# Kernel tuning notes

Hardware: AMD Instinct MI355X
Metric: run time of the kernel (lower is better)

The kernel has to match this reference:

```python
import math
import jax, jax.numpy as jnp
import numpy as np

BASE = 10000.0
SCALING_FACTOR = 1.0
ORIG_MAX_POS = 4096
BETA_FAST, BETA_SLOW = 32, 1
MSCALE = 0.707
MSCALE_ALL_DIM = 0.707


def _yarn_cos_sin(seq_len: int, dim: int):
    # DeepseekV3YarnRotaryEmbedding._set_cos_sin_cache, computed in numpy (constants)
    def corr_dim(num_rot):
        return dim * math.log(ORIG_MAX_POS / (num_rot * 2 * math.pi)) / (2 * math.log(BASE))
    low = max(math.floor(corr_dim(BETA_FAST)), 0)
    high = min(math.ceil(corr_dim(BETA_SLOW)), dim - 1)
    hi = high + 0.001 if low == high else high
    ramp = np.clip((np.arange(dim // 2, dtype=np.float32) - low) / (hi - low), 0.0, 1.0)
    inv_freq_mask = 1.0 - ramp
    freq_extra = 1.0 / BASE ** (np.arange(0, dim, 2, dtype=np.float32) / dim)
    freq_inter = freq_extra / SCALING_FACTOR
    inv_freq = freq_inter * (1.0 - inv_freq_mask) + freq_extra * inv_freq_mask
    t = np.arange(seq_len, dtype=np.float32)
    freqs = np.outer(t, inv_freq)
    def get_mscale(s, m):
        return 1.0 if s <= 1 else 0.1 * m * math.log(s) + 1.0
    _m = get_mscale(SCALING_FACTOR, MSCALE) / get_mscale(SCALING_FACTOR, MSCALE_ALL_DIM)
    emb = np.concatenate([freqs, freqs], axis=-1)  # [S, dim]
    return jnp.asarray(np.cos(emb) * _m), jnp.asarray(np.sin(emb) * _m)


def _rotate_half(x):
    x1, x2 = jnp.split(x, 2, axis=-1)
    return jnp.concatenate([-x2, x1], axis=-1)


def setup_inputs() -> dict:
    key = jax.random.key(0)
    ks = jax.random.split(key, 5)
    B, S, H, DN, DR, DV = 2, 2048, 16, 128, 64, 128
    return {
        "q_nope": jax.random.normal(ks[0], (B, S, H, DN), jnp.float32),
        "q_pe": jax.random.normal(ks[1], (B, S, H, DR), jnp.float32),
        "k_nope": jax.random.normal(ks[2], (B, S, H, DN), jnp.float32),
        "k_pe": jax.random.normal(ks[3], (B, S, 1, DR), jnp.float32),  # shared rope key head
        "v": jax.random.normal(ks[4], (B, S, H, DV), jnp.float32),
    }


def reference(q_nope, q_pe, k_nope, k_pe, v):
    B, S, H, DN = q_nope.shape
    DR = q_pe.shape[-1]
    sm_scale = (DN + DR) ** (-0.5)  # qk_head_dim**-0.5
    cos, sin = _yarn_cos_sin(S, DR)  # [S, DR]
    cos = cos[None, :, None, :]
    sin = sin[None, :, None, :]
    # decoupled RoPE on the rope slice (apply_rotary_pos_emb with position_ids=arange)
    qp = q_pe * cos + _rotate_half(q_pe) * sin              # [B,S,H,DR]
    kp = k_pe * cos + _rotate_half(k_pe) * sin              # [B,S,1,DR]
    kp = jnp.broadcast_to(kp, (B, S, H, DR))
    q = jnp.concatenate([q_nope, qp], axis=-1)              # [B,S,H,DN+DR]
    k = jnp.concatenate([k_nope, kp], axis=-1)
    # attention_ref: full fp32 logits, causal mask, lse*log2(e), softmax, PV
    logits = jnp.einsum('bmhd,bnhd->bhmn', q.astype(jnp.float32), k.astype(jnp.float32)) * sm_scale
    mask = jnp.arange(S)[:, None] >= jnp.arange(S)[None, :]  # qo_len == kv_len
    logits = jnp.where(mask[None, None], logits, -jnp.inf)
    lse = jnp.transpose(jax.scipy.special.logsumexp(logits, axis=-1), (0, 2, 1)) * math.log2(math.e)
    p = jax.nn.softmax(logits, axis=-1)
    o = jnp.einsum('bhmn,bnhd->bmhd', p, v.astype(jnp.float32))
    o = o.reshape(B * S, H, -1).astype(q_nope.dtype)        # [B*S, H, DV]
    return o, lse
```

## Files before the change

kernel.cpp:

```cpp
#include <hip/hip_runtime.h>
#include <hip/hip_bf16.h>
#include <math.h>

#define NB 2
#define SEQ 2048
#define NH 16
#define DNOPE 128
#define DROT 64
#define DVDIM 128
#define DQK 192
#define BM 64
#define BN 64

typedef __bf16 bf16x8_t __attribute__((ext_vector_type(8)));
typedef float f32x4_t __attribute__((ext_vector_type(4)));

#define LOG2_BASE_OVER_HALFDIM 0.41524101186092028f
#define KSL2 0.10412340175817158f

#define KBF_ELEMS   ((size_t)NB * NH * SEQ * DQK)
#define KPREP_BLOCKS 6144
#define VPREP_BLOCKS 1024

__global__ __launch_bounds__(256) void prep_kernel(
    const float* __restrict__ k_nope, const float* __restrict__ k_pe,
    const float* __restrict__ v, __bf16* __restrict__ Kbf,
    __bf16* __restrict__ Vtb) {
  __shared__ __bf16 T[64][130];
  const int bid = blockIdx.x;
  const int tid = threadIdx.x;
  if (bid < KPREP_BLOCKS) {
    int gid = bid * 256 + tid;
    size_t o8 = (size_t)gid * 8;
    int d0 = (int)(o8 % DQK);
    int rest = (int)(o8 / DQK);
    int s = rest & (SEQ - 1);
    int bh = rest >> 11;
    int h = bh & (NH - 1), b = bh >> 4;
    bf16x8_t o;
    if (d0 < DNOPE) {
      const float* p = k_nope + ((size_t)((b * SEQ + s) * NH + h)) * DNOPE + d0;
      float4 a = *(const float4*)p;
      float4 c = *(const float4*)(p + 4);
      o[0] = (__bf16)a.x; o[1] = (__bf16)a.y; o[2] = (__bf16)a.z; o[3] = (__bf16)a.w;
      o[4] = (__bf16)c.x; o[5] = (__bf16)c.y; o[6] = (__bf16)c.z; o[7] = (__bf16)c.w;
    } else {
      int dr0 = d0 - DNOPE;
      const float* p = k_pe + (size_t)(b * SEQ + s) * DROT;
#pragma unroll
      for (int j = 0; j < 8; ++j) {
        int dr = dr0 + j;
        int i = dr & 31;
        float invf = exp2f(-LOG2_BASE_OVER_HALFDIM * (float)i);
        float ang = (float)s * invf;
        float sn, cs; sincosf(ang, &sn, &cs);
        float x = p[dr];
        float oth = (dr < 32) ? -p[dr + 32] : p[dr - 32];
        o[j] = (__bf16)(x * cs + oth * sn);
      }
    }
    *(bf16x8_t*)&Kbf[o8] = o;
  } else {
    int vb = bid - KPREP_BLOCKS;
    const int s0 = (vb & 31) * 64, h = (vb >> 5) & (NH - 1), b = vb >> 9;
#pragma unroll
    for (int r = 0; r < 8; ++r) {
      int task = tid + r * 256;
      int srow = task >> 5, c4 = (task & 31) * 4;
      const float* p = v + ((size_t)((b * SEQ + s0 + srow) * NH + h)) * DVDIM + c4;
      float4 a = *(const float4*)p;
      T[srow][c4 + 0] = (__bf16)a.x; T[srow][c4 + 1] = (__bf16)a.y;
      T[srow][c4 + 2] = (__bf16)a.z; T[srow][c4 + 3] = (__bf16)a.w;
    }
    __syncthreads();
#pragma unroll
    for (int r = 0; r < 4; ++r) {
      int task = tid + r * 256;
      int dv = task >> 3, c8 = (task & 7) * 8;
      bf16x8_t o;
#pragma unroll
      for (int u = 0; u < 8; ++u) o[u] = T[c8 + u][dv];
      *(bf16x8_t*)&Vtb[((size_t)(b * NH + h) * DVDIM + dv) * SEQ + s0 + c8] = o;
    }
  }
}

__global__ __launch_bounds__(256, 2) void mla_fwd_kernel(
    const float* __restrict__ q_nope, const float* __restrict__ q_pe,
    const __bf16* __restrict__ Kbf, const __bf16* __restrict__ Vtb,
    float* __restrict__ out_o, float* __restrict__ out_lse) {
  __shared__ __bf16 Kl[BN * DQK];
  __shared__ __bf16 Vl[DVDIM * BN];
  __shared__ __bf16 Pl[4 * 16 * BN];
  __shared__ __bf16 Vx[16 * 72];

  const int bx = blockIdx.x, h = blockIdx.y, b = blockIdx.z;
  const int tid = threadIdx.x;
  const int w = tid >> 6, lane = tid & 63;
  const int col = lane & 15, quad = lane >> 4;
  const int swz = col & 7;
  const int e0 = quad ^ swz, e1 = (quad + 4) ^ swz;

  for (int i = tid; i < 16 * 72; i += 256)
    Vx[i] = (i < 64) ? (__bf16)1.0f : (__bf16)0.0f;

  const __bf16* Kslab = Kbf + (size_t)(b * NH + h) * SEQ * DQK;
  const __bf16* Vslab = Vtb + (size_t)(b * NH + h) * DVDIM * SEQ;

  int kofs[6];
#pragma unroll
  for (int r = 0; r < 6; ++r) {
    int L = r * 256 + tid;
    int n = L / 24, jj = L - n * 24;
    int jsrc = (jj & ~7) | ((jj & 7) ^ (n & 7));
    kofs[r] = n * DQK + jsrc * 8;
  }
  int vofs[4];
#pragma unroll
  for (int r = 0; r < 4; ++r) {
    int L = r * 256 + tid;
    int dv = L >> 3, jj = L & 7;
    vofs[r] = dv * SEQ + (jj ^ (dv & 7)) * 8;
  }

  __syncthreads();
  const bf16x8_t vxf0 = *(const bf16x8_t*)&Vx[col * 72 + quad * 8];
  const bf16x8_t vxf1 = *(const bf16x8_t*)&Vx[col * 72 + 32 + quad * 8];

  for (int half = 0; half < 2; ++half) {
    const int qt = half ? bx : (31 - bx);
    const int qb = qt * BM;
    const int mrow = qb + w * 16 + col;

    const float* qn = q_nope + (size_t)((b * SEQ + mrow) * NH + h) * DNOPE;
    const float* qp = q_pe   + (size_t)((b * SEQ + mrow) * NH + h) * DROT;
    bf16x8_t qfrag[6];
#pragma unroll
    for (int c = 0; c < 4; ++c) {
      const float* p = qn + c * 32 + quad * 8;
      float4 a = *(const float4*)p;
      float4 bq = *(const float4*)(p + 4);
      bf16x8_t f;
      f[0]=(__bf16)(a.x*KSL2);  f[1]=(__bf16)(a.y*KSL2);
      f[2]=(__bf16)(a.z*KSL2);  f[3]=(__bf16)(a.w*KSL2);
      f[4]=(__bf16)(bq.x*KSL2); f[5]=(__bf16)(bq.y*KSL2);
      f[6]=(__bf16)(bq.z*KSL2); f[7]=(__bf16)(bq.w*KSL2);
      qfrag[c] = f;
    }
    {
      const float* plo = qp + quad * 8;
      const float* phi = qp + 32 + quad * 8;
      float4 lo0 = *(const float4*)plo;
      float4 lo1 = *(const float4*)(plo + 4);
      float4 hi0 = *(const float4*)phi;
      float4 hi1 = *(const float4*)(phi + 4);
      float xl[8] = {lo0.x,lo0.y,lo0.z,lo0.w,lo1.x,lo1.y,lo1.z,lo1.w};
      float xh[8] = {hi0.x,hi0.y,hi0.z,hi0.w,hi1.x,hi1.y,hi1.z,hi1.w};
      bf16x8_t f4v, f5v;
#pragma unroll
      for (int j = 0; j < 8; ++j) {
        int i = quad * 8 + j;
        float invf = exp2f(-LOG2_BASE_OVER_HALFDIM * (float)i);
        float ang = (float)mrow * invf;
        float sn, cs; sincosf(ang, &sn, &cs);
        f4v[j] = (__bf16)((xl[j] * cs - xh[j] * sn) * KSL2);
        f5v[j] = (__bf16)((xh[j] * cs + xl[j] * sn) * KSL2);
      }
      qfrag[4] = f4v; qfrag[5] = f5v;
    }

    f32x4_t oacc[8];
#pragma unroll
    for (int i = 0; i < 8; ++i) oacc[i] = (f32x4_t){0.f, 0.f, 0.f, 0.f};
    f32x4_t lacc = (f32x4_t){0.f, 0.f, 0.f, 0.f};
    float m_run[4] = {-INFINITY, -INFINITY, -INFINITY, -INFINITY};

    bf16x8_t Kreg[6], Vreg[4];
#pragma unroll
    for (int r = 0; r < 6; ++r) Kreg[r] = *(const bf16x8_t*)(Kslab + kofs[r]);
#pragma unroll
    for (int r = 0; r < 4; ++r) Vreg[r] = *(const bf16x8_t*)(Vslab + vofs[r]);

    for (int it = 0; it <= qt; ++it) {
      __syncthreads();
#pragma unroll
      for (int r = 0; r < 6; ++r) *(bf16x8_t*)&Kl[(r * 256 + tid) * 8] = Kreg[r];
#pragma unroll
      for (int r = 0; r < 4; ++r) *(bf16x8_t*)&Vl[(r * 256 + tid) * 8] = Vreg[r];
      __syncthreads();
      if (it < qt) {
        const __bf16* Ksrc = Kslab + (size_t)(it + 1) * BN * DQK;
        const __bf16* Vsrc = Vslab + (it + 1) * BN;
#pragma unroll
        for (int r = 0; r < 6; ++r) Kreg[r] = *(const bf16x8_t*)(Ksrc + kofs[r]);
#pragma unroll
        for (int r = 0; r < 4; ++r) Vreg[r] = *(const bf16x8_t*)(Vsrc + vofs[r]);
      }

      f32x4_t sacc[4];
#pragma unroll
      for (int t = 0; t < 4; ++t) sacc[t] = (f32x4_t){0.f, 0.f, 0.f, 0.f};
#pragma unroll
      for (int t = 0; t < 4; ++t) {
        const __bf16* kr = &Kl[(t * 16 + col) * 24 * 8];
        sacc[t] = __builtin_amdgcn_mfma_f32_16x16x32_bf16(qfrag[0], *(const bf16x8_t*)&kr[e0 * 8], sacc[t], 0, 0, 0);
        sacc[t] = __builtin_amdgcn_mfma_f32_16x16x32_bf16(qfrag[1], *(const bf16x8_t*)&kr[e1 * 8], sacc[t], 0, 0, 0);
        sacc[t] = __builtin_amdgcn_mfma_f32_16x16x32_bf16(qfrag[2], *(const bf16x8_t*)&kr[64 + e0 * 8], sacc[t], 0, 0, 0);
        sacc[t] = __builtin_amdgcn_mfma_f32_16x16x32_bf16(qfrag[3], *(const bf16x8_t*)&kr[64 + e1 * 8], sacc[t], 0, 0, 0);
        sacc[t] = __builtin_amdgcn_mfma_f32_16x16x32_bf16(qfrag[4], *(const bf16x8_t*)&kr[128 + e0 * 8], sacc[t], 0, 0, 0);
        sacc[t] = __builtin_amdgcn_mfma_f32_16x16x32_bf16(qfrag[5], *(const bf16x8_t*)&kr[128 + e1 * 8], sacc[t], 0, 0, 0);
      }

      const bool diag = (it == qt);
      float pv[4][4];
      float alpha[4];
#pragma unroll
      for (int r = 0; r < 4; ++r) {
        float mx = -INFINITY;
#pragma unroll
        for (int t = 0; t < 4; ++t) {
          float sv = sacc[t][r];
          if (diag) {
            int nn = (qt << 6) + t * 16 + col;
            int mm = qb + w * 16 + quad * 4 + r;
            if (nn > mm) sv = -INFINITY;
          }
          pv[t][r] = sv;
          mx = fmaxf(mx, sv);
        }
        mx = fmaxf(mx, __shfl_xor(mx, 1, 64));
        mx = fmaxf(mx, __shfl_xor(mx, 2, 64));
        mx = fmaxf(mx, __shfl_xor(mx, 4, 64));
        mx = fmaxf(mx, __shfl_xor(mx, 8, 64));
        float mnew = fmaxf(m_run[r], mx);
        alpha[r] = exp2f(m_run[r] - mnew);
        m_run[r] = mnew;
#pragma unroll
        for (int t = 0; t < 4; ++t) pv[t][r] = exp2f(pv[t][r] - mnew);
      }
#pragma unroll
      for (int d = 0; d < 8; ++d) {
        f32x4_t o = oacc[d];
        o[0] *= alpha[0]; o[1] *= alpha[1]; o[2] *= alpha[2]; o[3] *= alpha[3];
        oacc[d] = o;
      }
      lacc[0] *= alpha[0]; lacc[1] *= alpha[1];
      lacc[2] *= alpha[2]; lacc[3] *= alpha[3];

      __bf16* Pw = &Pl[w * 16 * BN];
#pragma unroll
      for (int t = 0; t < 4; ++t)
#pragma unroll
        for (int r = 0; r < 4; ++r) {
          int row = quad * 4 + r;
          int j = t * 2 + (col >> 3);
          Pw[(row * 8 + (j ^ (row & 7))) * 8 + (col & 7)] = (__bf16)pv[t][r];
        }
      bf16x8_t pf0 = *(const bf16x8_t*)&Pw[(col * 8 + e0) * 8];
      bf16x8_t pf1 = *(const bf16x8_t*)&Pw[(col * 8 + e1) * 8];

#pragma unroll
      for (int d = 0; d < 8; ++d) {
        const __bf16* vr = &Vl[(d * 16 + col) * 64];
        bf16x8_t vf0 = *(const bf16x8_t*)&vr[e0 * 8];
        bf16x8_t vf1 = *(const bf16x8_t*)&vr[e1 * 8];
        oacc[d] = __builtin_amdgcn_mfma_f32_16x16x32_bf16(pf0, vf0, oacc[d], 0, 0, 0);
        oacc[d] = __builtin_amdgcn_mfma_f32_16x16x32_bf16(pf1, vf1, oacc[d], 0, 0, 0);
      }
      lacc = __builtin_amdgcn_mfma_f32_16x16x32_bf16(pf0, vxf0, lacc, 0, 0, 0);
      lacc = __builtin_amdgcn_mfma_f32_16x16x32_bf16(pf1, vxf1, lacc, 0, 0, 0);
    }

    float lr[4];
#pragma unroll
    for (int r = 0; r < 4; ++r) lr[r] = __shfl(lacc[r], lane & 48, 64);
    float inv_l[4];
#pragma unroll
    for (int r = 0; r < 4; ++r) inv_l[r] = 1.0f / lr[r];
#pragma unroll
    for (int d = 0; d < 8; ++d) {
#pragma unroll
      for (int r = 0; r < 4; ++r) {
        int mm = qb + w * 16 + quad * 4 + r;
        out_o[(size_t)((b * SEQ + mm) * NH + h) * DVDIM + d * 16 + col] = oacc[d][r] * inv_l[r];
      }
    }
    if (col < 4) {
      int r = col;
      int mm = qb + w * 16 + quad * 4 + r;
      out_lse[(size_t)(b * SEQ + mm) * NH + h] = m_run[r] + log2f(lr[r]);
    }
  }
}

extern "C" void kernel_launch(void* const* d_in, const int* in_sizes, int n_in,
                              void* d_out, int out_size, void* d_ws, size_t ws_size,
                              hipStream_t stream) {
  const float* q_nope = (const float*)d_in[0];
  const float* q_pe   = (const float*)d_in[1];
  const float* k_nope = (const float*)d_in[2];
  const float* k_pe   = (const float*)d_in[3];
  const float* v      = (const float*)d_in[4];
  float* out_o   = (float*)d_out;
  float* out_lse = out_o + (size_t)NB * SEQ * NH * DVDIM;

  __bf16* Kbf = (__bf16*)d_ws;
  __bf16* Vtb = Kbf + KBF_ELEMS;

  prep_kernel<<<dim3(KPREP_BLOCKS + VPREP_BLOCKS), dim3(256), 0, stream>>>(
      k_nope, k_pe, v, Kbf, Vtb);
  mla_fwd_kernel<<<dim3(16, NH, NB), dim3(256), 0, stream>>>(
      q_nope, q_pe, Kbf, Vtb, out_o, out_lse);
}
```

Measured before the change: 264.2 us.

## Double-buffer K/V via direct global-to-LDS loads with smaller KV tiles

The attention kernel now stages K/V tiles of 32 keys straight into LDS with global_load_lds into ping-pong buffers, replacing the register-staged copy with its two barriers per tile. The grid doubles to one query tile per block instead of pairing a short and a long tile per block. RoPE sincos switches to hardware sin/cos after range reduction, and LDS swizzling is dropped for V and P. The aim is to overlap memory traffic with MFMA work and cut register pressure, at the cost of possible LDS bank conflicts, more launched blocks with uneven causal work, and reduced sin/cos precision.

```diff
diff --git a/kernel.cpp b/kernel.cpp
--- a/kernel.cpp
+++ b/kernel.cpp
@@ -10,17 +10,33 @@
 #define DVDIM 128
 #define DQK 192
 #define BM 64
-#define BN 64
+#define BN 32
 
 typedef __bf16 bf16x8_t __attribute__((ext_vector_type(8)));
 typedef float f32x4_t __attribute__((ext_vector_type(4)));
 
 #define LOG2_BASE_OVER_HALFDIM 0.41524101186092028f
 #define KSL2 0.10412340175817158f
+#define INV2PI 0.15915494309189535f
 
 #define KBF_ELEMS   ((size_t)NB * NH * SEQ * DQK)
 #define KPREP_BLOCKS 6144
 #define VPREP_BLOCKS 1024
+
+__device__ __forceinline__ void fast_sincos(float ang, float* sn, float* cs) {
+  float rev = ang * INV2PI;
+  float r = rev - rintf(rev);
+  *sn = __builtin_amdgcn_sinf(r);
+  *cs = __builtin_amdgcn_cosf(r);
+}
+
+__device__ __forceinline__ void load_lds16(const __bf16* g, __bf16* l) {
+  __builtin_amdgcn_global_load_lds(
+      (const __attribute__((address_space(1))) unsigned int*)g,
+      (__attribute__((address_space(3))) unsigned int*)l, 16, 0, 0);
+}
+
+#define WAIT_VM0() __builtin_amdgcn_s_waitcnt(0x0F70)
 
 __global__ __launch_bounds__(256) void prep_kernel(
     const float* __restrict__ k_nope, const float* __restrict__ k_pe,
@@ -52,8 +68,8 @@
         int dr = dr0 + j;
         int i = dr & 31;
         float invf = exp2f(-LOG2_BASE_OVER_HALFDIM * (float)i);
-        float ang = (float)s * invf;
-        float sn, cs; sincosf(ang, &sn, &cs);
+        float sn, cs;
+        fast_sincos((float)s * invf, &sn, &cs);
         float x = p[dr];
         float oth = (dr < 32) ? -p[dr + 32] : p[dr - 32];
         o[j] = (__bf16)(x * cs + oth * sn);
@@ -89,207 +105,191 @@
     const float* __restrict__ q_nope, const float* __restrict__ q_pe,
     const __bf16* __restrict__ Kbf, const __bf16* __restrict__ Vtb,
     float* __restrict__ out_o, float* __restrict__ out_lse) {
-  __shared__ __bf16 Kl[BN * DQK];
-  __shared__ __bf16 Vl[DVDIM * BN];
-  __shared__ __bf16 Pl[4 * 16 * BN];
-  __shared__ __bf16 Vx[16 * 72];
-
-  const int bx = blockIdx.x, h = blockIdx.y, b = blockIdx.z;
+  __shared__ __bf16 KlA[BN * DQK];
+  __shared__ __bf16 KlB[BN * DQK];
+  __shared__ __bf16 VlA[DVDIM * BN];
+  __shared__ __bf16 VlB[DVDIM * BN];
+  __shared__ __bf16 Pl[4][16 * BN];
+  __shared__ __bf16 Vx[16 * BN];
+
+  const int qt = 31 - (int)blockIdx.x;
+  const int h = blockIdx.y, b = blockIdx.z;
+  const int qb = qt * BM;
   const int tid = threadIdx.x;
   const int w = tid >> 6, lane = tid & 63;
   const int col = lane & 15, quad = lane >> 4;
   const int swz = col & 7;
   const int e0 = quad ^ swz, e1 = (quad + 4) ^ swz;
 
-  for (int i = tid; i < 16 * 72; i += 256)
-    Vx[i] = (i < 64) ? (__bf16)1.0f : (__bf16)0.0f;
+  for (int i = tid; i < 16 * BN; i += 256)
+    Vx[i] = (i < BN) ? (__bf16)1.0f : (__bf16)0.0f;
 
   const __bf16* Kslab = Kbf + (size_t)(b * NH + h) * SEQ * DQK;
   const __bf16* Vslab = Vtb + (size_t)(b * NH + h) * DVDIM * SEQ;
 
-  int kofs[6];
-#pragma unroll
-  for (int r = 0; r < 6; ++r) {
+  int kofs[3];
+#pragma unroll
+  for (int r = 0; r < 3; ++r) {
     int L = r * 256 + tid;
     int n = L / 24, jj = L - n * 24;
     int jsrc = (jj & ~7) | ((jj & 7) ^ (n & 7));
     kofs[r] = n * DQK + jsrc * 8;
   }
-  int vofs[4];
-#pragma unroll
-  for (int r = 0; r < 4; ++r) {
+  int vofs[2];
+#pragma unroll
+  for (int r = 0; r < 2; ++r) {
     int L = r * 256 + tid;
-    int dv = L >> 3, jj = L & 7;
-    vofs[r] = dv * SEQ + (jj ^ (dv & 7)) * 8;
+    vofs[r] = (L >> 2) * SEQ + (L & 3) * 8;
   }
 
   __syncthreads();
-  const bf16x8_t vxf0 = *(const bf16x8_t*)&Vx[col * 72 + quad * 8];
-  const bf16x8_t vxf1 = *(const bf16x8_t*)&Vx[col * 72 + 32 + quad * 8];
-
-  for (int half = 0; half < 2; ++half) {
-    const int qt = half ? bx : (31 - bx);
-    const int qb = qt * BM;
-    const int mrow = qb + w * 16 + col;
-
-    const float* qn = q_nope + (size_t)((b * SEQ + mrow) * NH + h) * DNOPE;
-    const float* qp = q_pe   + (size_t)((b * SEQ + mrow) * NH + h) * DROT;
-    bf16x8_t qfrag[6];
-#pragma unroll
-    for (int c = 0; c < 4; ++c) {
-      const float* p = qn + c * 32 + quad * 8;
-      float4 a = *(const float4*)p;
-      float4 bq = *(const float4*)(p + 4);
-      bf16x8_t f;
-      f[0]=(__bf16)(a.x*KSL2);  f[1]=(__bf16)(a.y*KSL2);
-      f[2]=(__bf16)(a.z*KSL2);  f[3]=(__bf16)(a.w*KSL2);
-      f[4]=(__bf16)(bq.x*KSL2); f[5]=(__bf16)(bq.y*KSL2);
-      f[6]=(__bf16)(bq.z*KSL2); f[7]=(__bf16)(bq.w*KSL2);
-      qfrag[c] = f;
-    }
-    {
-      const float* plo = qp + quad * 8;
-      const float* phi = qp + 32 + quad * 8;
-      float4 lo0 = *(const float4*)plo;
-      float4 lo1 = *(const float4*)(plo + 4);
-      float4 hi0 = *(const float4*)phi;
-      float4 hi1 = *(const float4*)(phi + 4);
-      float xl[8] = {lo0.x,lo0.y,lo0.z,lo0.w,lo1.x,lo1.y,lo1.z,lo1.w};
-      float xh[8] = {hi0.x,hi0.y,hi0.z,hi0.w,hi1.x,hi1.y,hi1.z,hi1.w};
-      bf16x8_t f4v, f5v;
-#pragma unroll
-      for (int j = 0; j < 8; ++j) {
-        int i = quad * 8 + j;
-        float invf = exp2f(-LOG2_BASE_OVER_HALFDIM * (float)i);
-        float ang = (float)mrow * invf;
-        float sn, cs; sincosf(ang, &sn, &cs);
-        f4v[j] = (__bf16)((xl[j] * cs - xh[j] * sn) * KSL2);
-        f5v[j] = (__bf16)((xh[j] * cs + xl[j] * sn) * KSL2);
+  const bf16x8_t vxf = *(const bf16x8_t*)&Vx[col * BN + quad * 8];
+
+  auto stage = [&](int tile, __bf16* Kd, __bf16* Vd) {
+    const __bf16* Ks = Kslab + (size_t)tile * BN * DQK;
+    const __bf16* Vs = Vslab + tile * BN;
+#pragma unroll
+    for (int r = 0; r < 3; ++r) load_lds16(Ks + kofs[r], &Kd[(r * 256 + tid) * 8]);
+#pragma unroll
+    for (int r = 0; r < 2; ++r) load_lds16(Vs + vofs[r], &Vd[(r * 256 + tid) * 8]);
+  };
+
+  stage(0, KlA, VlA);
+
+  const int mrow = qb + w * 16 + col;
+  const float* qn = q_nope + (size_t)((b * SEQ + mrow) * NH + h) * DNOPE;
+  const float* qp = q_pe   + (size_t)((b * SEQ + mrow) * NH + h) * DROT;
+  bf16x8_t qfrag[6];
+#pragma unroll
+  for (int c = 0; c < 4; ++c) {
+    const float* p = qn + c * 32 + quad * 8;
+    float4 a = *(const float4*)p;
+    float4 bq = *(const float4*)(p + 4);
+    bf16x8_t f;
+    f[0]=(__bf16)(a.x*KSL2);  f[1]=(__bf16)(a.y*KSL2);
+    f[2]=(__bf16)(a.z*KSL2);  f[3]=(__bf16)(a.w*KSL2);
+    f[4]=(__bf16)(bq.x*KSL2); f[5]=(__bf16)(bq.y*KSL2);
+    f[6]=(__bf16)(bq.z*KSL2); f[7]=(__bf16)(bq.w*KSL2);
+    qfrag[c] = f;
+  }
+  {
+    const float* plo = qp + quad * 8;
+    const float* phi = qp + 32 + quad * 8;
+    float4 lo0 = *(const float4*)plo;
+    float4 lo1 = *(const float4*)(plo + 4);
+    float4 hi0 = *(const float4*)phi;
+    float4 hi1 = *(const float4*)(phi + 4);
+    float xl[8] = {lo0.x,lo0.y,lo0.z,lo0.w,lo1.x,lo1.y,lo1.z,lo1.w};
+    float xh[8] = {hi0.x,hi0.y,hi0.z,hi0.w,hi1.x,hi1.y,hi1.z,hi1.w};
+    bf16x8_t f4v, f5v;
+#pragma unroll
+    for (int j = 0; j < 8; ++j) {
+      int i = quad * 8 + j;
+      float invf = exp2f(-LOG2_BASE_OVER_HALFDIM * (float)i);
+      float sn, cs;
+      fast_sincos((float)mrow * invf, &sn, &cs);
+      f4v[j] = (__bf16)((xl[j] * cs - xh[j] * sn) * KSL2);
+      f5v[j] = (__bf16)((xh[j] * cs + xl[j] * sn) * KSL2);
+    }
+    qfrag[4] = f4v; qfrag[5] = f5v;
+  }
+
+  f32x4_t oacc[8];
+#pragma unroll
+  for (int i = 0; i < 8; ++i) oacc[i] = (f32x4_t){0.f, 0.f, 0.f, 0.f};
+  f32x4_t lacc = (f32x4_t){0.f, 0.f, 0.f, 0.f};
+  float m_run[4] = {-INFINITY, -INFINITY, -INFINITY, -INFINITY};
+
+  auto compute = [&](const __bf16* Kt, const __bf16* Vt, int kb) {
+    f32x4_t sacc[2];
+#pragma unroll
+    for (int t = 0; t < 2; ++t) sacc[t] = (f32x4_t){0.f, 0.f, 0.f, 0.f};
+#pragma unroll
+    for (int t = 0; t < 2; ++t) {
+      const __bf16* kr = &Kt[(t * 16 + col) * DQK];
+      sacc[t] = __builtin_amdgcn_mfma_f32_16x16x32_bf16(qfrag[0], *(const bf16x8_t*)&kr[e0 * 8], sacc[t], 0, 0, 0);
+      sacc[t] = __builtin_amdgcn_mfma_f32_16x16x32_bf16(qfrag[1], *(const bf16x8_t*)&kr[e1 * 8], sacc[t], 0, 0, 0);
+      sacc[t] = __builtin_amdgcn_mfma_f32_16x16x32_bf16(qfrag[2], *(const bf16x8_t*)&kr[64 + e0 * 8], sacc[t], 0, 0, 0);
+      sacc[t] = __builtin_amdgcn_mfma_f32_16x16x32_bf16(qfrag[3], *(const bf16x8_t*)&kr[64 + e1 * 8], sacc[t], 0, 0, 0);
+      sacc[t] = __builtin_amdgcn_mfma_f32_16x16x32_bf16(qfrag[4], *(const bf16x8_t*)&kr[128 + e0 * 8], sacc[t], 0, 0, 0);
+      sacc[t] = __builtin_amdgcn_mfma_f32_16x16x32_bf16(qfrag[5], *(const bf16x8_t*)&kr[128 + e1 * 8], sacc[t], 0, 0, 0);
+    }
+
+    const bool mk = (kb + BN - 1 > qb + w * 16);
+    float pv0[4], pv1[4], alpha[4];
+#pragma unroll
+    for (int r = 0; r < 4; ++r) {
+      float s0 = sacc[0][r], s1 = sacc[1][r];
+      if (mk) {
+        int mm = qb + w * 16 + quad * 4 + r;
+        if (kb + col > mm)      s0 = -INFINITY;
+        if (kb + 16 + col > mm) s1 = -INFINITY;
       }
-      qfrag[4] = f4v; qfrag[5] = f5v;
-    }
-
-    f32x4_t oacc[8];
-#pragma unroll
-    for (int i = 0; i < 8; ++i) oacc[i] = (f32x4_t){0.f, 0.f, 0.f, 0.f};
-    f32x4_t lacc = (f32x4_t){0.f, 0.f, 0.f, 0.f};
-    float m_run[4] = {-INFINITY, -INFINITY, -INFINITY, -INFINITY};
-
-    bf16x8_t Kreg[6], Vreg[4];
-#pragma unroll
-    for (int r = 0; r < 6; ++r) Kreg[r] = *(const bf16x8_t*)(Kslab + kofs[r]);
-#pragma unroll
-    for (int r = 0; r < 4; ++r) Vreg[r] = *(const bf16x8_t*)(Vslab + vofs[r]);
-
-    for (int it = 0; it <= qt; ++it) {
-      __syncthreads();
-#pragma unroll
-      for (int r = 0; r < 6; ++r) *(bf16x8_t*)&Kl[(r * 256 + tid) * 8] = Kreg[r];
-#pragma unroll
-      for (int r = 0; r < 4; ++r) *(bf16x8_t*)&Vl[(r * 256 + tid) * 8] = Vreg[r];
-      __syncthreads();
-      if (it < qt) {
-        const __bf16* Ksrc = Kslab + (size_t)(it + 1) * BN * DQK;
-        const __bf16* Vsrc = Vslab + (it + 1) * BN;
-#pragma unroll
-        for (int r = 0; r < 6; ++r) Kreg[r] = *(const bf16x8_t*)(Ksrc + kofs[r]);
-#pragma unroll
-        for (int r = 0; r < 4; ++r) Vreg[r] = *(const bf16x8_t*)(Vsrc + vofs[r]);
-      }
-
-      f32x4_t sacc[4];
-#pragma unroll
-      for (int t = 0; t < 4; ++t) sacc[t] = (f32x4_t){0.f, 0.f, 0.f, 0.f};
-#pragma unroll
-      for (int t = 0; t < 4; ++t) {
-        const __bf16* kr = &Kl[(t * 16 + col) * 24 * 8];
-        sacc[t] = __builtin_amdgcn_mfma_f32_16x16x32_bf16(qfrag[0], *(const bf16x8_t*)&kr[e0 * 8], sacc[t], 0, 0, 0);
-        sacc[t] = __builtin_amdgcn_mfma_f32_16x16x32_bf16(qfrag[1], *(const bf16x8_t*)&kr[e1 * 8], sacc[t], 0, 0, 0);
-        sacc[t] = __builtin_amdgcn_mfma_f32_16x16x32_bf16(qfrag[2], *(const bf16x8_t*)&kr[64 + e0 * 8], sacc[t], 0, 0, 0);
-        sacc[t] = __builtin_amdgcn_mfma_f32_16x16x32_bf16(qfrag[3], *(const bf16x8_t*)&kr[64 + e1 * 8], sacc[t], 0, 0, 0);
-        sacc[t] = __builtin_amdgcn_mfma_f32_16x16x32_bf16(qfrag[4], *(const bf16x8_t*)&kr[128 + e0 * 8], sacc[t], 0, 0, 0);
-        sacc[t] = __builtin_amdgcn_mfma_f32_16x16x32_bf16(qfrag[5], *(const bf16x8_t*)&kr[128 + e1 * 8], sacc[t], 0, 0, 0);
-      }
-
-      const bool diag = (it == qt);
-      float pv[4][4];
-      float alpha[4];
-#pragma unroll
-      for (int r = 0; r < 4; ++r) {
-        float mx = -INFINITY;
-#pragma unroll
-        for (int t = 0; t < 4; ++t) {
-          float sv = sacc[t][r];
-          if (diag) {
-            int nn = (qt << 6) + t * 16 + col;
-            int mm = qb + w * 16 + quad * 4 + r;
-            if (nn > mm) sv = -INFINITY;
-          }
-          pv[t][r] = sv;
-          mx = fmaxf(mx, sv);
-        }
-        mx = fmaxf(mx, __shfl_xor(mx, 1, 64));
-        mx = fmaxf(mx, __shfl_xor(mx, 2, 64));
-        mx = fmaxf(mx, __shfl_xor(mx, 4, 64));
-        mx = fmaxf(mx, __shfl_xor(mx, 8, 64));
-        float mnew = fmaxf(m_run[r], mx);
-        alpha[r] = exp2f(m_run[r] - mnew);
-        m_run[r] = mnew;
-#pragma unroll
-        for (int t = 0; t < 4; ++t) pv[t][r] = exp2f(pv[t][r] - mnew);
-      }
-#pragma unroll
-      for (int d = 0; d < 8; ++d) {
-        f32x4_t o = oacc[d];
-        o[0] *= alpha[0]; o[1] *= alpha[1]; o[2] *= alpha[2]; o[3] *= alpha[3];
-        oacc[d] = o;
-      }
-      lacc[0] *= alpha[0]; lacc[1] *= alpha[1];
-      lacc[2] *= alpha[2]; lacc[3] *= alpha[3];
-
-      __bf16* Pw = &Pl[w * 16 * BN];
-#pragma unroll
-      for (int t = 0; t < 4; ++t)
-#pragma unroll
-        for (int r = 0; r < 4; ++r) {
-          int row = quad * 4 + r;
-          int j = t * 2 + (col >> 3);
-          Pw[(row * 8 + (j ^ (row & 7))) * 8 + (col & 7)] = (__bf16)pv[t][r];
-        }
-      bf16x8_t pf0 = *(const bf16x8_t*)&Pw[(col * 8 + e0) * 8];
-      bf16x8_t pf1 = *(const bf16x8_t*)&Pw[(col * 8 + e1) * 8];
-
-#pragma unroll
-      for (int d = 0; d < 8; ++d) {
-        const __bf16* vr = &Vl[(d * 16 + col) * 64];
-        bf16x8_t vf0 = *(const bf16x8_t*)&vr[e0 * 8];
-        bf16x8_t vf1 = *(const bf16x8_t*)&vr[e1 * 8];
-        oacc[d] = __builtin_amdgcn_mfma_f32_16x16x32_bf16(pf0, vf0, oacc[d], 0, 0, 0);
-        oacc[d] = __builtin_amdgcn_mfma_f32_16x16x32_bf16(pf1, vf1, oacc[d], 0, 0, 0);
-      }
-      lacc = __builtin_amdgcn_mfma_f32_16x16x32_bf16(pf0, vxf0, lacc, 0, 0, 0);
-      lacc = __builtin_amdgcn_mfma_f32_16x16x32_bf16(pf1, vxf1, lacc, 0, 0, 0);
-    }
-
-    float lr[4];
-#pragma unroll
-    for (int r = 0; r < 4; ++r) lr[r] = __shfl(lacc[r], lane & 48, 64);
-    float inv_l[4];
-#pragma unroll
-    for (int r = 0; r < 4; ++r) inv_l[r] = 1.0f / lr[r];
+      float mx = fmaxf(s0, s1);
+      mx = fmaxf(mx, __shfl_xor(mx, 1, 64));
+      mx = fmaxf(mx, __shfl_xor(mx, 2, 64));
+      mx = fmaxf(mx, __shfl_xor(mx, 4, 64));
+      mx = fmaxf(mx, __shfl_xor(mx, 8, 64));
+      float mnew = fmaxf(m_run[r], mx);
+      alpha[r] = exp2f(m_run[r] - mnew);
+      m_run[r] = mnew;
+      pv0[r] = exp2f(s0 - mnew);
+      pv1[r] = exp2f(s1 - mnew);
+    }
 #pragma unroll
     for (int d = 0; d < 8; ++d) {
-#pragma unroll
-      for (int r = 0; r < 4; ++r) {
-        int mm = qb + w * 16 + quad * 4 + r;
-        out_o[(size_t)((b * SEQ + mm) * NH + h) * DVDIM + d * 16 + col] = oacc[d][r] * inv_l[r];
-      }
-    }
-    if (col < 4) {
-      int r = col;
+      f32x4_t o = oacc[d];
+      o[0] *= alpha[0]; o[1] *= alpha[1]; o[2] *= alpha[2]; o[3] *= alpha[3];
+      oacc[d] = o;
+    }
+    lacc[0] *= alpha[0]; lacc[1] *= alpha[1];
+    lacc[2] *= alpha[2]; lacc[3] *= alpha[3];
+
+    __bf16* Pw = Pl[w];
+#pragma unroll
+    for (int r = 0; r < 4; ++r) {
+      Pw[(quad * 4 + r) * BN + col]      = (__bf16)pv0[r];
+      Pw[(quad * 4 + r) * BN + 16 + col] = (__bf16)pv1[r];
+    }
+    bf16x8_t pf = *(const bf16x8_t*)&Pw[col * BN + quad * 8];
+
+#pragma unroll
+    for (int d = 0; d < 8; ++d) {
+      bf16x8_t vf = *(const bf16x8_t*)&Vt[(d * 16 + col) * BN + quad * 8];
+      oacc[d] = __builtin_amdgcn_mfma_f32_16x16x32_bf16(pf, vf, oacc[d], 0, 0, 0);
+    }
+    lacc = __builtin_amdgcn_mfma_f32_16x16x32_bf16(pf, vxf, lacc, 0, 0, 0);
+  };
+
+  for (int it2 = 0; it2 <= qt; ++it2) {
+    WAIT_VM0();
+    __syncthreads();
+    stage(2 * it2 + 1, KlB, VlB);
+    compute(KlA, VlA, (2 * it2) * BN);
+    WAIT_VM0();
+    __syncthreads();
+    if (it2 < qt) stage(2 * it2 + 2, KlA, VlA);
+    compute(KlB, VlB, (2 * it2 + 1) * BN);
+  }
+
+  float lr[4];
+#pragma unroll
+  for (int r = 0; r < 4; ++r) lr[r] = __shfl(lacc[r], lane & 48, 64);
+  float inv_l[4];
+#pragma unroll
+  for (int r = 0; r < 4; ++r) inv_l[r] = 1.0f / lr[r];
+#pragma unroll
+  for (int d = 0; d < 8; ++d) {
+#pragma unroll
+    for (int r = 0; r < 4; ++r) {
       int mm = qb + w * 16 + quad * 4 + r;
-      out_lse[(size_t)(b * SEQ + mm) * NH + h] = m_run[r] + log2f(lr[r]);
-    }
+      out_o[(size_t)((b * SEQ + mm) * NH + h) * DVDIM + d * 16 + col] = oacc[d][r] * inv_l[r];
+    }
+  }
+  if (col < 4) {
+    int r = col;
+    int mm = qb + w * 16 + quad * 4 + r;
+    out_lse[(size_t)(b * SEQ + mm) * NH + h] = m_run[r] + log2f(lr[r]);
   }
 }
 
@@ -309,6 +309,6 @@
 
   prep_kernel<<<dim3(KPREP_BLOCKS + VPREP_BLOCKS), dim3(256), 0, stream>>>(
       k_nope, k_pe, v, Kbf, Vtb);
-  mla_fwd_kernel<<<dim3(16, NH, NB), dim3(256), 0, stream>>>(
+  mla_fwd_kernel<<<dim3(32, NH, NB), dim3(256), 0, stream>>>(
       q_nope, q_pe, Kbf, Vtb, out_o, out_lse);
 }
```

New measurement: 387.9 us. 1.47x slower.
